# Optimization experiments

Measured on AMD Instinct MI355X. Metric: run time of the kernel, lower is better.

Reference implementation:

```python
import jax, jax.numpy as jnp
import numpy as np

B, S, D = 2, 2048, 1024
H = 16
HD = D // H  # 64
THETA = 10000.0


def apply_rope(x, positions, theta):
    # x: (b, h, s, hd); positions: (s,)
    hd = x.shape[-1]
    inv_freq = theta ** (-jnp.arange(0, hd, 2, dtype=jnp.float32) / hd)  # (hd/2,)
    angles = positions.astype(jnp.float32)[:, None] * inv_freq[None, :]  # (s, hd/2)
    cos, sin = jnp.cos(angles), jnp.sin(angles)
    x1 = x[..., 0::2]
    x2 = x[..., 1::2]
    r1 = x1 * cos - x2 * sin
    r2 = x1 * sin + x2 * cos
    out = jnp.stack([r1, r2], axis=-1).reshape(x.shape)
    return out.astype(x.dtype)


def setup_inputs() -> dict:
    key = jax.random.key(0)
    ks = jax.random.split(key, 5)
    scale = 1.0 / np.sqrt(D)
    return {
        "in_features": jax.random.normal(ks[0], (B, S, D), dtype=jnp.float32),
        "token_positions": jnp.arange(S, dtype=jnp.int32),
        "Wq": jax.random.normal(ks[1], (D, D), dtype=jnp.float32) * scale,
        "Wk": jax.random.normal(ks[2], (D, D), dtype=jnp.float32) * scale,
        "Wv": jax.random.normal(ks[3], (D, D), dtype=jnp.float32) * scale,
        "Wo": jax.random.normal(ks[4], (D, D), dtype=jnp.float32) * scale,
    }


def reference(in_features, token_positions, Wq, Wk, Wv, Wo):
    b, s, d = in_features.shape
    h, hd = H, HD
    # bias-free linear: y = x @ W.T  (W is (out, in))
    q = in_features @ Wq.T
    k = in_features @ Wk.T
    v = in_features @ Wv.T
    # (b, s, h*hd) -> (b, h, s, hd)
    split = lambda t: t.reshape(b, s, h, hd).transpose(0, 2, 1, 3)
    q, k, v = split(q), split(k), split(v)
    q = apply_rope(q, token_positions, THETA)
    k = apply_rope(k, token_positions, THETA)
    scores = jnp.einsum("bhid,bhjd->bhij", q, k) / jnp.sqrt(jnp.asarray(hd, dtype=q.dtype))
    causal = jnp.triu(jnp.ones((s, s), dtype=bool), k=1)
    scores = jnp.where(causal, -jnp.inf, scores)
    attn = jax.nn.softmax(scores, axis=-1)
    out = jnp.einsum("bhij,bhjd->bhid", attn, v)
    out = out.transpose(0, 2, 1, 3).reshape(b, s, d)
    return out @ Wo.T
```

## Files before the change

kernel.cpp:

```cpp
#include <hip/hip_runtime.h>
#include <math.h>

#define NUM_HEADS 16
#define HEAD_DIM 64

typedef __bf16 bf16x8 __attribute__((ext_vector_type(8)));
typedef short shortx4 __attribute__((ext_vector_type(4)));
typedef float floatx4 __attribute__((ext_vector_type(4)));

__device__ __forceinline__ unsigned short f2b(float f) {
  unsigned int u = __float_as_uint(f);
  u += 0x7fffu + ((u >> 16) & 1u);
  return (unsigned short)(u >> 16);
}
__device__ __forceinline__ float b2f(unsigned short s) {
  return __uint_as_float(((unsigned int)s) << 16);
}

__device__ __forceinline__ void async16(const void* g, void* l) {
  __builtin_amdgcn_global_load_lds(
      (const __attribute__((address_space(1))) unsigned int*)g,
      (__attribute__((address_space(3))) unsigned int*)l, 16, 0, 0);
}

__global__ void cvt_f32_bf16(const float* __restrict__ in,
                             unsigned short* __restrict__ out, int n4) {
  int i = blockIdx.x * 256 + threadIdx.x;
  if (i < n4) {
    float4 v = ((const float4*)in)[i];
    ushort4 o;
    o.x = f2b(v.x); o.y = f2b(v.y); o.z = f2b(v.z); o.w = f2b(v.w);
    ((ushort4*)out)[i] = o;
  }
}

__global__ void cvt_w4(const float* __restrict__ w0, const float* __restrict__ w1,
                       const float* __restrict__ w2, const float* __restrict__ w3,
                       unsigned short* o0, unsigned short* o1,
                       unsigned short* o2, unsigned short* o3, int n4) {
  int i = blockIdx.x * 256 + threadIdx.x;
  if (i >= n4) return;
  const float* in = (blockIdx.y == 0) ? w0 : (blockIdx.y == 1) ? w1
                   : (blockIdx.y == 2) ? w2 : w3;
  unsigned short* out = (blockIdx.y == 0) ? o0 : (blockIdx.y == 1) ? o1
                       : (blockIdx.y == 2) ? o2 : o3;
  float4 v = ((const float4*)in)[i];
  ushort4 o;
  o.x = f2b(v.x); o.y = f2b(v.y); o.z = f2b(v.z); o.w = f2b(v.w);
  ((ushort4*)out)[i] = o;
}

__global__ void build_rope_tab(const int* __restrict__ pos,
                               float* __restrict__ tab, int total) {
  int t = blockIdx.x * 256 + threadIdx.x;
  if (t >= total) return;
  int i = t & 31, s = t >> 5;
  float inv = expf(-0.28782313662425575f * (float)i);
  float ang = (float)pos[s] * inv;
  float sn, cs;
  sincosf(ang, &sn, &cs);
  tab[t * 2] = cs;
  tab[t * 2 + 1] = sn;
}

template <int MODE>
__global__ __launch_bounds__(256, 2)
void gemm_bt(const unsigned short* __restrict__ A,
             const unsigned short* __restrict__ B0,
             const unsigned short* __restrict__ B1,
             const unsigned short* __restrict__ B2,
             void* out0v, void* out1v, void* out2v,
             const float* __restrict__ ctab,
             int M, int N, int K, int S) {
  __shared__ unsigned short As[128 * 32];
  __shared__ unsigned short Bs[128 * 32];
  const int tid = threadIdx.x;
  const int lane = tid & 63;
  const int w = tid >> 6;
  const int lane16 = lane & 15;
  const int g = lane >> 4;
  const int wm = w >> 1, wn = w & 1;
  const int m0 = blockIdx.y * 128;
  const int n0 = blockIdx.x * 128;
  const unsigned short* Bp = (blockIdx.z == 0) ? B0 : (blockIdx.z == 1 ? B1 : B2);

  const floatx4 vzero = {0.f, 0.f, 0.f, 0.f};
  floatx4 acc[4][4];
#pragma unroll
  for (int i = 0; i < 4; i++)
#pragma unroll
    for (int j = 0; j < 4; j++) acc[i][j] = vzero;

  const int ar = lane >> 2;
  const int ac = (lane & 3) * 8;

  for (int k0 = 0; k0 < K; k0 += 32) {
#pragma unroll
    for (int c = 0; c < 2; c++) {
      int chunk = w * 2 + c;
      async16(A  + (size_t)(m0 + chunk * 16 + ar) * K + k0 + ac, As + chunk * 512);
      async16(Bp + (size_t)(n0 + chunk * 16 + ar) * K + k0 + ac, Bs + chunk * 512);
    }
    __syncthreads();
    bf16x8 a[4], b[4];
#pragma unroll
    for (int mt = 0; mt < 4; mt++)
      a[mt] = *(const bf16x8*)&As[(wm * 64 + mt * 16 + lane16) * 32 + g * 8];
#pragma unroll
    for (int nt = 0; nt < 4; nt++)
      b[nt] = *(const bf16x8*)&Bs[(wn * 64 + nt * 16 + lane16) * 32 + g * 8];
#pragma unroll
    for (int mt = 0; mt < 4; mt++)
#pragma unroll
      for (int nt = 0; nt < 4; nt++)
        acc[mt][nt] = __builtin_amdgcn_mfma_f32_16x16x32_bf16(b[nt], a[mt], acc[mt][nt], 0, 0, 0);
    __syncthreads();
  }

  if (MODE == 0) {
    unsigned short* outp = (unsigned short*)((blockIdx.z == 0) ? out0v
                              : (blockIdx.z == 1 ? out1v : out2v));
    const bool dorope = (blockIdx.z < 2);
    const float qs = (blockIdx.z == 0) ? 0.125f : 1.0f;
#pragma unroll
    for (int mt = 0; mt < 4; mt++) {
      int m = m0 + wm * 64 + mt * 16 + lane16;
      int bb = m / S, s = m - bb * S;
      const float* crow = ctab + (size_t)s * 64;
#pragma unroll
      for (int nt = 0; nt < 4; nt++) {
        int n = n0 + wn * 64 + nt * 16 + g * 4;
        int h = n >> 6, dl = n & 63;
        floatx4 v = acc[mt][nt];
        if (dorope) {
          float4 cs = *(const float4*)&crow[dl];
          float r0 = (v[0] * cs.x - v[1] * cs.y) * qs;
          float r1 = (v[0] * cs.y + v[1] * cs.x) * qs;
          float r2 = (v[2] * cs.z - v[3] * cs.w) * qs;
          float r3 = (v[2] * cs.w + v[3] * cs.z) * qs;
          v[0] = r0; v[1] = r1; v[2] = r2; v[3] = r3;
        }
        shortx4 st;
#pragma unroll
        for (int r = 0; r < 4; r++) st[r] = (short)f2b(v[r]);
        *(shortx4*)&outp[(((size_t)(bb * NUM_HEADS + h) * S + s) << 6) + dl] = st;
      }
    }
  } else {
    float* outp = (float*)out0v;
#pragma unroll
    for (int mt = 0; mt < 4; mt++) {
      int m = m0 + wm * 64 + mt * 16 + lane16;
#pragma unroll
      for (int nt = 0; nt < 4; nt++) {
        int n = n0 + wn * 64 + nt * 16 + g * 4;
        *(floatx4*)&outp[(size_t)m * N + n] = acc[mt][nt];
      }
    }
  }
}

__global__ __launch_bounds__(256, 4)
void transpose_v(const unsigned short* __restrict__ V,
                 unsigned short* __restrict__ Vt, int S) {
  __shared__ unsigned short t[64 * 72];
  const int tid = threadIdx.x;
  const int lane = tid & 63;
  const int w = tid >> 6;
  const int bh = blockIdx.y;
  const int s0 = blockIdx.x * 64;
  const size_t ibase = (size_t)bh * S * 64;
#pragma unroll
  for (int c = 0; c < 2; ++c) {
    int ch = c * 4 + w;
    union { uint4 v; unsigned short u[8]; } vb;
    vb.v = *(const uint4*)&V[ibase + (size_t)(s0 + lane) * 64 + ch * 8];
#pragma unroll
    for (int e = 0; e < 8; ++e) t[(ch * 8 + e) * 72 + lane] = vb.u[e];
  }
  __syncthreads();
  const size_t obase = (size_t)bh * 64 * S;
#pragma unroll
  for (int c = 0; c < 2; ++c) {
    int idx = c * 256 + tid;
    int d = idx >> 3, sch = idx & 7;
    *(uint4*)&Vt[obase + (size_t)d * S + s0 + sch * 8] = *(const uint4*)&t[d * 72 + sch * 8];
  }
}

__global__ __launch_bounds__(256, 4)
void flash_attn4(const unsigned short* __restrict__ Q,
                 const unsigned short* __restrict__ Kv,
                 const unsigned short* __restrict__ Vt,
                 unsigned short* __restrict__ Oattn, int S) {
  __shared__ unsigned short Ks[2 * 4096];
  __shared__ unsigned short Vs[2 * 4096];
  const int tid = threadIdx.x;
  const int lane = tid & 63;
  const int w = tid >> 6;
  const int lane16 = lane & 15;
  const int g = lane >> 4;
  const int sw = lane16 & 7;
  const int qt = gridDim.x - 1 - blockIdx.x;
  const int bh = blockIdx.y;
  const int b = bh >> 4, h = bh & 15;
  const size_t kbase = (size_t)bh * S * HEAD_DIM;
  const unsigned short* Kbase = Kv + kbase;
  const unsigned short* Vtbase = Vt + (size_t)bh * HEAD_DIM * S;
  const int qrow0 = qt * 64 + w * 16;

  bf16x8 qf0, qf1;
  {
    const unsigned short* qp = Q + kbase + (size_t)(qrow0 + lane16) * HEAD_DIM + g * 8;
    qf0 = *(const bf16x8*)qp;
    qf1 = *(const bf16x8*)(qp + 32);
  }

  const int ci0 = w * 64 + lane;
  const int ci1 = ci0 + 256;
  const int r0 = ci0 >> 3, j0 = (ci0 & 7) ^ (r0 & 7);
  const int r1 = ci1 >> 3, j1 = (ci1 & 7) ^ (r1 & 7);
  const unsigned short* kS0 = Kbase + r0 * HEAD_DIM + j0 * 8;
  const unsigned short* kS1 = Kbase + r1 * HEAD_DIM + j1 * 8;
  const unsigned short* vS0 = Vtbase + (size_t)r0 * S + j0 * 8;
  const unsigned short* vS1 = Vtbase + (size_t)r1 * S + j1 * 8;
  unsigned short* kD0 = Ks + ci0 * 8;
  unsigned short* kD1 = Ks + ci1 * 8;
  unsigned short* vD0 = Vs + ci0 * 8;
  unsigned short* vD1 = Vs + ci1 * 8;

  auto stage = [&](int t, int bi) {
    int koff = t * 4096;
    int voff = t * 64;
    int doff = bi * 4096;
    async16(kS0 + koff, kD0 + doff);
    async16(kS1 + koff, kD1 + doff);
    async16(vS0 + voff, vD0 + doff);
    async16(vS1 + voff, vD1 + doff);
  };

  const floatx4 vzero = {0.f, 0.f, 0.f, 0.f};
  floatx4 oacc[4];
#pragma unroll
  for (int i = 0; i < 4; i++) oacc[i] = vzero;
  float l_i = 0.f;

  stage(0, 0);
  __syncthreads();

  for (int t = 0; t <= qt; ++t) {
    const int bi = t & 1;
    if (t < qt) stage(t + 1, bi ^ 1);
    const unsigned short* Kb_ = Ks + bi * 4096;
    const unsigned short* Vb_ = Vs + bi * 4096;

    floatx4 sc[4];
#pragma unroll
    for (int c = 0; c < 4; ++c) {
      int r = c * 16 + lane16;
      bf16x8 kf0 = *(const bf16x8*)&Kb_[(r * 8 + (g ^ sw)) * 8];
      bf16x8 kf1 = *(const bf16x8*)&Kb_[(r * 8 + ((4 + g) ^ sw)) * 8];
      floatx4 s = vzero;
      s = __builtin_amdgcn_mfma_f32_16x16x32_bf16(kf0, qf0, s, 0, 0, 0);
      s = __builtin_amdgcn_mfma_f32_16x16x32_bf16(kf1, qf1, s, 0, 0, 0);
      sc[c] = s;
    }
    if (t == qt) {
      const int i = qrow0 + lane16;
      const int jb = t * 64;
#pragma unroll
      for (int c = 0; c < 4; ++c)
#pragma unroll
        for (int r = 0; r < 4; ++r)
          if (jb + c * 16 + g * 4 + r > i) sc[c][r] = -INFINITY;
    }
    shortx4 pc[4];
#pragma unroll
    for (int c = 0; c < 4; ++c) {
      float p0 = __expf(sc[c][0]);
      float p1 = __expf(sc[c][1]);
      float p2 = __expf(sc[c][2]);
      float p3 = __expf(sc[c][3]);
      l_i += (p0 + p1) + (p2 + p3);
      union { unsigned int u[2]; shortx4 s4; } pu;
      pu.u[0] = __builtin_amdgcn_perm(__float_as_uint(p1), __float_as_uint(p0), 0x07060302u);
      pu.u[1] = __builtin_amdgcn_perm(__float_as_uint(p3), __float_as_uint(p2), 0x07060302u);
      pc[c] = pu.s4;
    }
#pragma unroll
    for (int nt = 0; nt < 4; ++nt) {
      int rv = nt * 16 + lane16;
#pragma unroll
      for (int c = 0; c < 4; ++c) {
        shortx4 vf = *(const shortx4*)&Vb_[(rv * 8 + ((c * 2 + (g >> 1)) ^ sw)) * 8 + (g & 1) * 4];
        oacc[nt] = __builtin_amdgcn_mfma_f32_16x16x16bf16_1k(vf, pc[c], oacc[nt], 0, 0, 0);
      }
    }
    __syncthreads();
  }

  l_i += __shfl_xor(l_i, 16, 64);
  l_i += __shfl_xor(l_i, 32, 64);
  {
    float inv = 1.0f / l_i;
    int srow = qrow0 + lane16;
    size_t rowb = ((size_t)b * S + srow) * 1024 + h * 64;
#pragma unroll
    for (int nt = 0; nt < 4; ++nt) {
      shortx4 st;
#pragma unroll
      for (int r = 0; r < 4; ++r) st[r] = (short)f2b(oacc[nt][r] * inv);
      *(shortx4*)&Oattn[rowb + nt * 16 + g * 4] = st;
    }
  }
}

extern "C" void kernel_launch(void* const* d_in, const int* in_sizes, int n_in,
                              void* d_out, int out_size, void* d_ws, size_t ws_size,
                              hipStream_t stream) {
  const float* x  = (const float*)d_in[0];
  const int*  pos = (const int*)d_in[1];
  const float* wq = (const float*)d_in[2];
  const float* wk = (const float*)d_in[3];
  const float* wv = (const float*)d_in[4];
  const float* wo = (const float*)d_in[5];

  const int D = 1024;
  const int S = in_sizes[1];
  const int M = in_sizes[0] / D;
  const int B = M / S;
  const int BH = B * NUM_HEADS;

  char* wsb = (char*)d_ws;
  size_t off = 0;
  auto alloc = [&](size_t bytes) {
    char* p = wsb + off;
    off += (bytes + 255) & ~(size_t)255;
    return p;
  };
  unsigned short* Xb   = (unsigned short*)alloc((size_t)M * D * 2);
  unsigned short* Wqb  = (unsigned short*)alloc((size_t)D * D * 2);
  unsigned short* Wkb  = (unsigned short*)alloc((size_t)D * D * 2);
  unsigned short* Wvb  = (unsigned short*)alloc((size_t)D * D * 2);
  unsigned short* Wob  = (unsigned short*)alloc((size_t)D * D * 2);
  unsigned short* Qb   = (unsigned short*)alloc((size_t)M * D * 2);
  unsigned short* Kb   = (unsigned short*)alloc((size_t)M * D * 2);
  unsigned short* Vb   = (unsigned short*)alloc((size_t)M * D * 2);
  unsigned short* Attn = (unsigned short*)alloc((size_t)M * D * 2);
  float*          Ctab = (float*)alloc((size_t)S * 32 * 2 * 4);
  unsigned short* Vtb  = Xb;
  (void)ws_size;

  {
    int n4 = M * D / 4;
    cvt_f32_bf16<<<dim3((n4 + 255) / 256), 256, 0, stream>>>(x, Xb, n4);
    int w4 = D * D / 4;
    cvt_w4<<<dim3((w4 + 255) / 256, 4), 256, 0, stream>>>(
        wq, wk, wv, wo, Wqb, Wkb, Wvb, Wob, w4);
    int tt = S * 32;
    build_rope_tab<<<dim3((tt + 255) / 256), 256, 0, stream>>>(pos, Ctab, tt);
  }
  gemm_bt<0><<<dim3(D / 128, M / 128, 3), 256, 0, stream>>>(
      Xb, Wqb, Wkb, Wvb, Qb, Kb, Vb, Ctab, M, D, D, S);
  transpose_v<<<dim3(S / 64, BH), 256, 0, stream>>>(Vb, Vtb, S);
  flash_attn4<<<dim3(S / 64, BH), 256, 0, stream>>>(Qb, Kb, Vtb, Attn, S);
  gemm_bt<1><<<dim3(D / 128, M / 128, 1), 256, 0, stream>>>(
      Attn, Wob, Wob, Wob, d_out, d_out, d_out, Ctab, M, D, D, S);
}
```

Measured before the change: 204.2 us.

## Fuse prep kernels, double-buffer GEMM with K=64 stages, widen attention blocks

Merges the input, weight and RoPE-table preparation kernels into one launch. The projection GEMM now stages 64-wide K tiles into double-buffered LDS, prefetching the next tile while computing the current one, which halves the number of barriers. The attention kernel moves to 512-thread blocks covering 128 query rows, so each K/V tile load is shared by eight waves. That wider block costs extra causal-masking work near the diagonal, more LDS per block and possible occupancy changes.

New measurement: 219.5 us. 1.08x slower.

```diff
diff --git a/kernel.cpp b/kernel.cpp
--- a/kernel.cpp
+++ b/kernel.cpp
@@ -13,9 +13,6 @@
   u += 0x7fffu + ((u >> 16) & 1u);
   return (unsigned short)(u >> 16);
 }
-__device__ __forceinline__ float b2f(unsigned short s) {
-  return __uint_as_float(((unsigned int)s) << 16);
-}
 
 __device__ __forceinline__ void async16(const void* g, void* l) {
   __builtin_amdgcn_global_load_lds(
@@ -23,44 +20,42 @@
       (__attribute__((address_space(3))) unsigned int*)l, 16, 0, 0);
 }
 
-__global__ void cvt_f32_bf16(const float* __restrict__ in,
-                             unsigned short* __restrict__ out, int n4) {
-  int i = blockIdx.x * 256 + threadIdx.x;
-  if (i < n4) {
-    float4 v = ((const float4*)in)[i];
-    ushort4 o;
-    o.x = f2b(v.x); o.y = f2b(v.y); o.z = f2b(v.z); o.w = f2b(v.w);
-    ((ushort4*)out)[i] = o;
-  }
-}
-
-__global__ void cvt_w4(const float* __restrict__ w0, const float* __restrict__ w1,
-                       const float* __restrict__ w2, const float* __restrict__ w3,
-                       unsigned short* o0, unsigned short* o1,
-                       unsigned short* o2, unsigned short* o3, int n4) {
-  int i = blockIdx.x * 256 + threadIdx.x;
-  if (i >= n4) return;
-  const float* in = (blockIdx.y == 0) ? w0 : (blockIdx.y == 1) ? w1
-                   : (blockIdx.y == 2) ? w2 : w3;
-  unsigned short* out = (blockIdx.y == 0) ? o0 : (blockIdx.y == 1) ? o1
-                       : (blockIdx.y == 2) ? o2 : o3;
+__device__ __forceinline__ void cvt4(const float* in, unsigned short* out, int i) {
   float4 v = ((const float4*)in)[i];
   ushort4 o;
   o.x = f2b(v.x); o.y = f2b(v.y); o.z = f2b(v.z); o.w = f2b(v.w);
   ((ushort4*)out)[i] = o;
 }
 
-__global__ void build_rope_tab(const int* __restrict__ pos,
-                               float* __restrict__ tab, int total) {
-  int t = blockIdx.x * 256 + threadIdx.x;
-  if (t >= total) return;
-  int i = t & 31, s = t >> 5;
-  float inv = expf(-0.28782313662425575f * (float)i);
-  float ang = (float)pos[s] * inv;
-  float sn, cs;
-  sincosf(ang, &sn, &cs);
-  tab[t * 2] = cs;
-  tab[t * 2 + 1] = sn;
+__global__ void prep(const float* __restrict__ x,
+                     const float* __restrict__ w0, const float* __restrict__ w1,
+                     const float* __restrict__ w2, const float* __restrict__ w3,
+                     const int* __restrict__ pos,
+                     unsigned short* Xb, unsigned short* o0, unsigned short* o1,
+                     unsigned short* o2, unsigned short* o3,
+                     float* __restrict__ tab, int w4, int ntab) {
+  int i = blockIdx.x * 256 + threadIdx.x;
+  int z = blockIdx.y;
+  if (z == 0) {
+#pragma unroll
+    for (int rep = 0; rep < 4; ++rep) cvt4(x, Xb, rep * 262144 + i);
+  } else if (z <= 4) {
+    if (i < w4) {
+      const float* in = (z == 1) ? w0 : (z == 2) ? w1 : (z == 3) ? w2 : w3;
+      unsigned short* out = (z == 1) ? o0 : (z == 2) ? o1 : (z == 3) ? o2 : o3;
+      cvt4(in, out, i);
+    }
+  } else {
+    if (i < ntab) {
+      int fi = i & 31, s = i >> 5;
+      float inv = expf(-0.28782313662425575f * (float)fi);
+      float ang = (float)pos[s] * inv;
+      float sn, cs;
+      sincosf(ang, &sn, &cs);
+      tab[i * 2] = cs;
+      tab[i * 2 + 1] = sn;
+    }
+  }
 }
 
 template <int MODE>
@@ -72,8 +67,8 @@
              void* out0v, void* out1v, void* out2v,
              const float* __restrict__ ctab,
              int M, int N, int K, int S) {
-  __shared__ unsigned short As[128 * 32];
-  __shared__ unsigned short Bs[128 * 32];
+  __shared__ unsigned short As[2 * 8192];
+  __shared__ unsigned short Bs[2 * 8192];
   const int tid = threadIdx.x;
   const int lane = tid & 63;
   const int w = tid >> 6;
@@ -93,27 +88,50 @@
 
   const int ar = lane >> 2;
   const int ac = (lane & 3) * 8;
-
-  for (int k0 = 0; k0 < K; k0 += 32) {
-#pragma unroll
-    for (int c = 0; c < 2; c++) {
-      int chunk = w * 2 + c;
-      async16(A  + (size_t)(m0 + chunk * 16 + ar) * K + k0 + ac, As + chunk * 512);
-      async16(Bp + (size_t)(n0 + chunk * 16 + ar) * K + k0 + ac, Bs + chunk * 512);
-    }
-    __syncthreads();
-    bf16x8 a[4], b[4];
-#pragma unroll
-    for (int mt = 0; mt < 4; mt++)
-      a[mt] = *(const bf16x8*)&As[(wm * 64 + mt * 16 + lane16) * 32 + g * 8];
-#pragma unroll
-    for (int nt = 0; nt < 4; nt++)
-      b[nt] = *(const bf16x8*)&Bs[(wn * 64 + nt * 16 + lane16) * 32 + g * 8];
-#pragma unroll
-    for (int mt = 0; mt < 4; mt++)
+  const unsigned short* aS[4];
+  const unsigned short* bS[4];
+  unsigned short* aD[4];
+  unsigned short* bD[4];
+#pragma unroll
+  for (int q = 0; q < 4; ++q) {
+    int ci = w * 4 + q, rc = ci >> 1, kh = ci & 1;
+    aS[q] = A  + (size_t)(m0 + rc * 16 + ar) * K + kh * 32 + ac;
+    bS[q] = Bp + (size_t)(n0 + rc * 16 + ar) * K + kh * 32 + ac;
+    aD[q] = As + ci * 512;
+    bD[q] = Bs + ci * 512;
+  }
+  auto stage = [&](int k0, int bi) {
+    int doff = bi * 8192;
+#pragma unroll
+    for (int q = 0; q < 4; ++q) {
+      async16(aS[q] + k0, aD[q] + doff);
+      async16(bS[q] + k0, bD[q] + doff);
+    }
+  };
+
+  stage(0, 0);
+  __syncthreads();
+
+  for (int k0 = 0; k0 < K; k0 += 64) {
+    const int bi = (k0 >> 6) & 1;
+    if (k0 + 64 < K) stage(k0 + 64, bi ^ 1);
+    const unsigned short* Ab = As + bi * 8192;
+    const unsigned short* Bb = Bs + bi * 8192;
+#pragma unroll
+    for (int kh = 0; kh < 2; ++kh) {
+      bf16x8 a[4], b[4];
+#pragma unroll
+      for (int mt = 0; mt < 4; mt++)
+        a[mt] = *(const bf16x8*)&Ab[((wm * 4 + mt) * 2 + kh) * 512 + lane16 * 32 + g * 8];
 #pragma unroll
       for (int nt = 0; nt < 4; nt++)
-        acc[mt][nt] = __builtin_amdgcn_mfma_f32_16x16x32_bf16(b[nt], a[mt], acc[mt][nt], 0, 0, 0);
+        b[nt] = *(const bf16x8*)&Bb[((wn * 4 + nt) * 2 + kh) * 512 + lane16 * 32 + g * 8];
+#pragma unroll
+      for (int mt = 0; mt < 4; mt++)
+#pragma unroll
+        for (int nt = 0; nt < 4; nt++)
+          acc[mt][nt] = __builtin_amdgcn_mfma_f32_16x16x32_bf16(b[nt], a[mt], acc[mt][nt], 0, 0, 0);
+    }
     __syncthreads();
   }
 
@@ -188,8 +206,8 @@
   }
 }
 
-__global__ __launch_bounds__(256, 4)
-void flash_attn4(const unsigned short* __restrict__ Q,
+__global__ __launch_bounds__(512, 2)
+void flash_attn7(const unsigned short* __restrict__ Q,
                  const unsigned short* __restrict__ Kv,
                  const unsigned short* __restrict__ Vt,
                  unsigned short* __restrict__ Oattn, int S) {
@@ -201,42 +219,33 @@
   const int lane16 = lane & 15;
   const int g = lane >> 4;
   const int sw = lane16 & 7;
-  const int qt = gridDim.x - 1 - blockIdx.x;
+  const int qb = gridDim.x - 1 - blockIdx.x;
   const int bh = blockIdx.y;
   const int b = bh >> 4, h = bh & 15;
   const size_t kbase = (size_t)bh * S * HEAD_DIM;
   const unsigned short* Kbase = Kv + kbase;
   const unsigned short* Vtbase = Vt + (size_t)bh * HEAD_DIM * S;
-  const int qrow0 = qt * 64 + w * 16;
+  const int base = qb * 128 + w * 16;
+  const int diag = (base >> 6);
+  const int tmax = 2 * qb + 1;
 
   bf16x8 qf0, qf1;
   {
-    const unsigned short* qp = Q + kbase + (size_t)(qrow0 + lane16) * HEAD_DIM + g * 8;
+    const unsigned short* qp = Q + kbase + (size_t)(base + lane16) * HEAD_DIM + g * 8;
     qf0 = *(const bf16x8*)qp;
     qf1 = *(const bf16x8*)(qp + 32);
   }
 
-  const int ci0 = w * 64 + lane;
-  const int ci1 = ci0 + 256;
-  const int r0 = ci0 >> 3, j0 = (ci0 & 7) ^ (r0 & 7);
-  const int r1 = ci1 >> 3, j1 = (ci1 & 7) ^ (r1 & 7);
-  const unsigned short* kS0 = Kbase + r0 * HEAD_DIM + j0 * 8;
-  const unsigned short* kS1 = Kbase + r1 * HEAD_DIM + j1 * 8;
-  const unsigned short* vS0 = Vtbase + (size_t)r0 * S + j0 * 8;
-  const unsigned short* vS1 = Vtbase + (size_t)r1 * S + j1 * 8;
-  unsigned short* kD0 = Ks + ci0 * 8;
-  unsigned short* kD1 = Ks + ci1 * 8;
-  unsigned short* vD0 = Vs + ci0 * 8;
-  unsigned short* vD1 = Vs + ci1 * 8;
+  const int ci = tid;
+  const int r0 = ci >> 3, j0 = (ci & 7) ^ (r0 & 7);
+  const unsigned short* kS = Kbase + r0 * HEAD_DIM + j0 * 8;
+  const unsigned short* vS = Vtbase + (size_t)r0 * S + j0 * 8;
+  unsigned short* kD = Ks + ci * 8;
+  unsigned short* vD = Vs + ci * 8;
 
   auto stage = [&](int t, int bi) {
-    int koff = t * 4096;
-    int voff = t * 64;
-    int doff = bi * 4096;
-    async16(kS0 + koff, kD0 + doff);
-    async16(kS1 + koff, kD1 + doff);
-    async16(vS0 + voff, vD0 + doff);
-    async16(vS1 + voff, vD1 + doff);
+    async16(kS + t * 4096, kD + bi * 4096);
+    async16(vS + t * 64, vD + bi * 4096);
   };
 
   const floatx4 vzero = {0.f, 0.f, 0.f, 0.f};
@@ -248,9 +257,9 @@
   stage(0, 0);
   __syncthreads();
 
-  for (int t = 0; t <= qt; ++t) {
+  for (int t = 0; t <= tmax; ++t) {
     const int bi = t & 1;
-    if (t < qt) stage(t + 1, bi ^ 1);
+    if (t < tmax) stage(t + 1, bi ^ 1);
     const unsigned short* Kb_ = Ks + bi * 4096;
     const unsigned short* Vb_ = Vs + bi * 4096;
 
@@ -265,8 +274,8 @@
       s = __builtin_amdgcn_mfma_f32_16x16x32_bf16(kf1, qf1, s, 0, 0, 0);
       sc[c] = s;
     }
-    if (t == qt) {
-      const int i = qrow0 + lane16;
+    if (t >= diag) {
+      const int i = base + lane16;
       const int jb = t * 64;
 #pragma unroll
       for (int c = 0; c < 4; ++c)
@@ -303,7 +312,7 @@
   l_i += __shfl_xor(l_i, 32, 64);
   {
     float inv = 1.0f / l_i;
-    int srow = qrow0 + lane16;
+    int srow = base + lane16;
     size_t rowb = ((size_t)b * S + srow) * 1024 + h * 64;
 #pragma unroll
     for (int nt = 0; nt < 4; ++nt) {
@@ -352,18 +361,16 @@
   (void)ws_size;
 
   {
-    int n4 = M * D / 4;
-    cvt_f32_bf16<<<dim3((n4 + 255) / 256), 256, 0, stream>>>(x, Xb, n4);
     int w4 = D * D / 4;
-    cvt_w4<<<dim3((w4 + 255) / 256, 4), 256, 0, stream>>>(
-        wq, wk, wv, wo, Wqb, Wkb, Wvb, Wob, w4);
-    int tt = S * 32;
-    build_rope_tab<<<dim3((tt + 255) / 256), 256, 0, stream>>>(pos, Ctab, tt);
+    int ntab = S * 32;
+    prep<<<dim3(1024, 6), 256, 0, stream>>>(x, wq, wk, wv, wo, pos,
+                                            Xb, Wqb, Wkb, Wvb, Wob, Ctab,
+                                            w4, ntab);
   }
   gemm_bt<0><<<dim3(D / 128, M / 128, 3), 256, 0, stream>>>(
       Xb, Wqb, Wkb, Wvb, Qb, Kb, Vb, Ctab, M, D, D, S);
   transpose_v<<<dim3(S / 64, BH), 256, 0, stream>>>(Vb, Vtb, S);
-  flash_attn4<<<dim3(S / 64, BH), 256, 0, stream>>>(Qb, Kb, Vtb, Attn, S);
+  flash_attn7<<<dim3(S / 128, BH), 512, 0, stream>>>(Qb, Kb, Vtb, Attn, S);
   gemm_bt<1><<<dim3(D / 128, M / 128, 1), 256, 0, stream>>>(
       Attn, Wob, Wob, Wob, d_out, d_out, d_out, Ctab, M, D, D, S);
 }
```

## Fuse prep kernels, write V transposed from GEMM, use 64-row tiles for output GEMM

Applied to the files above, without the earlier changes.

Folds the input/weight bf16 conversions and RoPE table build into a single prep kernel to cut launch count. The QKV GEMM epilogue now writes V directly in transposed (d-major) layout, which removes the separate transpose kernel, at the cost of scalar strided 2-byte stores. The output projection GEMM uses 64-row tiles with higher occupancy bounds so more blocks cover the 256 CUs.

After: 192.8 us. 5.6% less time.

```diff
diff --git a/kernel.cpp b/kernel.cpp
--- a/kernel.cpp
+++ b/kernel.cpp
@@ -13,9 +13,6 @@
   u += 0x7fffu + ((u >> 16) & 1u);
   return (unsigned short)(u >> 16);
 }
-__device__ __forceinline__ float b2f(unsigned short s) {
-  return __uint_as_float(((unsigned int)s) << 16);
-}
 
 __device__ __forceinline__ void async16(const void* g, void* l) {
   __builtin_amdgcn_global_load_lds(
@@ -23,48 +20,48 @@
       (__attribute__((address_space(3))) unsigned int*)l, 16, 0, 0);
 }
 
-__global__ void cvt_f32_bf16(const float* __restrict__ in,
-                             unsigned short* __restrict__ out, int n4) {
-  int i = blockIdx.x * 256 + threadIdx.x;
-  if (i < n4) {
-    float4 v = ((const float4*)in)[i];
-    ushort4 o;
-    o.x = f2b(v.x); o.y = f2b(v.y); o.z = f2b(v.z); o.w = f2b(v.w);
-    ((ushort4*)out)[i] = o;
-  }
-}
-
-__global__ void cvt_w4(const float* __restrict__ w0, const float* __restrict__ w1,
-                       const float* __restrict__ w2, const float* __restrict__ w3,
-                       unsigned short* o0, unsigned short* o1,
-                       unsigned short* o2, unsigned short* o3, int n4) {
-  int i = blockIdx.x * 256 + threadIdx.x;
-  if (i >= n4) return;
-  const float* in = (blockIdx.y == 0) ? w0 : (blockIdx.y == 1) ? w1
-                   : (blockIdx.y == 2) ? w2 : w3;
-  unsigned short* out = (blockIdx.y == 0) ? o0 : (blockIdx.y == 1) ? o1
-                       : (blockIdx.y == 2) ? o2 : o3;
+__device__ __forceinline__ void cvt4(const float* in, unsigned short* out, int i) {
   float4 v = ((const float4*)in)[i];
   ushort4 o;
   o.x = f2b(v.x); o.y = f2b(v.y); o.z = f2b(v.z); o.w = f2b(v.w);
   ((ushort4*)out)[i] = o;
 }
 
-__global__ void build_rope_tab(const int* __restrict__ pos,
-                               float* __restrict__ tab, int total) {
-  int t = blockIdx.x * 256 + threadIdx.x;
-  if (t >= total) return;
-  int i = t & 31, s = t >> 5;
-  float inv = expf(-0.28782313662425575f * (float)i);
-  float ang = (float)pos[s] * inv;
-  float sn, cs;
-  sincosf(ang, &sn, &cs);
-  tab[t * 2] = cs;
-  tab[t * 2 + 1] = sn;
-}
-
-template <int MODE>
-__global__ __launch_bounds__(256, 2)
+__global__ void prep(const float* __restrict__ x,
+                     const float* __restrict__ w0, const float* __restrict__ w1,
+                     const float* __restrict__ w2, const float* __restrict__ w3,
+                     const int* __restrict__ pos,
+                     unsigned short* Xb, unsigned short* o0, unsigned short* o1,
+                     unsigned short* o2, unsigned short* o3,
+                     float* __restrict__ tab, int xq, int w4, int ntab) {
+  int i = blockIdx.x * 256 + threadIdx.x;
+  int z = blockIdx.y;
+  if (z == 0) {
+    if (i < xq) {
+#pragma unroll
+      for (int rep = 0; rep < 4; ++rep) cvt4(x, Xb, rep * xq + i);
+    }
+  } else if (z <= 4) {
+    if (i < w4) {
+      const float* in = (z == 1) ? w0 : (z == 2) ? w1 : (z == 3) ? w2 : w3;
+      unsigned short* out = (z == 1) ? o0 : (z == 2) ? o1 : (z == 3) ? o2 : o3;
+      cvt4(in, out, i);
+    }
+  } else {
+    if (i < ntab) {
+      int fi = i & 31, s = i >> 5;
+      float inv = expf(-0.28782313662425575f * (float)fi);
+      float ang = (float)pos[s] * inv;
+      float sn, cs;
+      sincosf(ang, &sn, &cs);
+      tab[i * 2] = cs;
+      tab[i * 2 + 1] = sn;
+    }
+  }
+}
+
+template <int MODE, int MT>
+__global__ __launch_bounds__(256, MODE == 1 ? 4 : 2)
 void gemm_bt(const unsigned short* __restrict__ A,
              const unsigned short* __restrict__ B0,
              const unsigned short* __restrict__ B1,
@@ -72,22 +69,23 @@
              void* out0v, void* out1v, void* out2v,
              const float* __restrict__ ctab,
              int M, int N, int K, int S) {
-  __shared__ unsigned short As[128 * 32];
-  __shared__ unsigned short Bs[128 * 32];
+  __shared__ unsigned short As[(MT / 16) * 512];
+  __shared__ unsigned short Bs[8 * 512];
   const int tid = threadIdx.x;
   const int lane = tid & 63;
   const int w = tid >> 6;
   const int lane16 = lane & 15;
   const int g = lane >> 4;
   const int wm = w >> 1, wn = w & 1;
-  const int m0 = blockIdx.y * 128;
+  const int m0 = blockIdx.y * MT;
   const int n0 = blockIdx.x * 128;
   const unsigned short* Bp = (blockIdx.z == 0) ? B0 : (blockIdx.z == 1 ? B1 : B2);
+  constexpr int MTILES = MT / 32;
 
   const floatx4 vzero = {0.f, 0.f, 0.f, 0.f};
-  floatx4 acc[4][4];
-#pragma unroll
-  for (int i = 0; i < 4; i++)
+  floatx4 acc[MTILES][4];
+#pragma unroll
+  for (int i = 0; i < MTILES; i++)
 #pragma unroll
     for (int j = 0; j < 4; j++) acc[i][j] = vzero;
 
@@ -95,22 +93,28 @@
   const int ac = (lane & 3) * 8;
 
   for (int k0 = 0; k0 < K; k0 += 32) {
-#pragma unroll
-    for (int c = 0; c < 2; c++) {
-      int chunk = w * 2 + c;
-      async16(A  + (size_t)(m0 + chunk * 16 + ar) * K + k0 + ac, As + chunk * 512);
-      async16(Bp + (size_t)(n0 + chunk * 16 + ar) * K + k0 + ac, Bs + chunk * 512);
+    if constexpr (MT == 128) {
+#pragma unroll
+      for (int c = 0; c < 2; c++) {
+        int chunk = w * 2 + c;
+        async16(A  + (size_t)(m0 + chunk * 16 + ar) * K + k0 + ac, As + chunk * 512);
+        async16(Bp + (size_t)(n0 + chunk * 16 + ar) * K + k0 + ac, Bs + chunk * 512);
+      }
+    } else {
+      async16(A  + (size_t)(m0 + w * 16 + ar) * K + k0 + ac, As + w * 512);
+      async16(Bp + (size_t)(n0 + w * 16 + ar) * K + k0 + ac, Bs + w * 512);
+      async16(Bp + (size_t)(n0 + (w + 4) * 16 + ar) * K + k0 + ac, Bs + (w + 4) * 512);
     }
     __syncthreads();
-    bf16x8 a[4], b[4];
-#pragma unroll
-    for (int mt = 0; mt < 4; mt++)
-      a[mt] = *(const bf16x8*)&As[(wm * 64 + mt * 16 + lane16) * 32 + g * 8];
+    bf16x8 a[MTILES], b[4];
+#pragma unroll
+    for (int mt = 0; mt < MTILES; mt++)
+      a[mt] = *(const bf16x8*)&As[(wm * (MT / 2) + mt * 16 + lane16) * 32 + g * 8];
 #pragma unroll
     for (int nt = 0; nt < 4; nt++)
       b[nt] = *(const bf16x8*)&Bs[(wn * 64 + nt * 16 + lane16) * 32 + g * 8];
 #pragma unroll
-    for (int mt = 0; mt < 4; mt++)
+    for (int mt = 0; mt < MTILES; mt++)
 #pragma unroll
       for (int nt = 0; nt < 4; nt++)
         acc[mt][nt] = __builtin_amdgcn_mfma_f32_16x16x32_bf16(b[nt], a[mt], acc[mt][nt], 0, 0, 0);
@@ -118,73 +122,59 @@
   }
 
   if (MODE == 0) {
-    unsigned short* outp = (unsigned short*)((blockIdx.z == 0) ? out0v
-                              : (blockIdx.z == 1 ? out1v : out2v));
-    const bool dorope = (blockIdx.z < 2);
-    const float qs = (blockIdx.z == 0) ? 0.125f : 1.0f;
-#pragma unroll
-    for (int mt = 0; mt < 4; mt++) {
-      int m = m0 + wm * 64 + mt * 16 + lane16;
-      int bb = m / S, s = m - bb * S;
-      const float* crow = ctab + (size_t)s * 64;
-#pragma unroll
-      for (int nt = 0; nt < 4; nt++) {
-        int n = n0 + wn * 64 + nt * 16 + g * 4;
-        int h = n >> 6, dl = n & 63;
-        floatx4 v = acc[mt][nt];
-        if (dorope) {
+    if (blockIdx.z < 2) {
+      unsigned short* outp = (unsigned short*)((blockIdx.z == 0) ? out0v : out1v);
+      const float qs = (blockIdx.z == 0) ? 0.125f : 1.0f;
+#pragma unroll
+      for (int mt = 0; mt < MTILES; mt++) {
+        int m = m0 + wm * (MT / 2) + mt * 16 + lane16;
+        int bb = m / S, s = m - bb * S;
+        const float* crow = ctab + (size_t)s * 64;
+#pragma unroll
+        for (int nt = 0; nt < 4; nt++) {
+          int n = n0 + wn * 64 + nt * 16 + g * 4;
+          int h = n >> 6, dl = n & 63;
+          floatx4 v = acc[mt][nt];
           float4 cs = *(const float4*)&crow[dl];
           float r0 = (v[0] * cs.x - v[1] * cs.y) * qs;
           float r1 = (v[0] * cs.y + v[1] * cs.x) * qs;
           float r2 = (v[2] * cs.z - v[3] * cs.w) * qs;
           float r3 = (v[2] * cs.w + v[3] * cs.z) * qs;
-          v[0] = r0; v[1] = r1; v[2] = r2; v[3] = r3;
+          shortx4 st;
+          st[0] = (short)f2b(r0); st[1] = (short)f2b(r1);
+          st[2] = (short)f2b(r2); st[3] = (short)f2b(r3);
+          *(shortx4*)&outp[(((size_t)(bb * NUM_HEADS + h) * S + s) << 6) + dl] = st;
         }
-        shortx4 st;
-#pragma unroll
-        for (int r = 0; r < 4; r++) st[r] = (short)f2b(v[r]);
-        *(shortx4*)&outp[(((size_t)(bb * NUM_HEADS + h) * S + s) << 6) + dl] = st;
+      }
+    } else {
+      unsigned short* outp = (unsigned short*)out2v;
+#pragma unroll
+      for (int mt = 0; mt < MTILES; mt++) {
+        int m = m0 + wm * (MT / 2) + mt * 16 + lane16;
+        int bb = m / S, s = m - bb * S;
+#pragma unroll
+        for (int nt = 0; nt < 4; nt++) {
+          int n = n0 + wn * 64 + nt * 16 + g * 4;
+          int bh = bb * NUM_HEADS + (n >> 6);
+          int dl = n & 63;
+          size_t dbase = ((size_t)bh * 64 + dl) * S + s;
+#pragma unroll
+          for (int r = 0; r < 4; r++)
+            outp[dbase + (size_t)r * S] = f2b(acc[mt][nt][r]);
+        }
       }
     }
   } else {
     float* outp = (float*)out0v;
 #pragma unroll
-    for (int mt = 0; mt < 4; mt++) {
-      int m = m0 + wm * 64 + mt * 16 + lane16;
+    for (int mt = 0; mt < MTILES; mt++) {
+      int m = m0 + wm * (MT / 2) + mt * 16 + lane16;
 #pragma unroll
       for (int nt = 0; nt < 4; nt++) {
         int n = n0 + wn * 64 + nt * 16 + g * 4;
         *(floatx4*)&outp[(size_t)m * N + n] = acc[mt][nt];
       }
     }
-  }
-}
-
-__global__ __launch_bounds__(256, 4)
-void transpose_v(const unsigned short* __restrict__ V,
-                 unsigned short* __restrict__ Vt, int S) {
-  __shared__ unsigned short t[64 * 72];
-  const int tid = threadIdx.x;
-  const int lane = tid & 63;
-  const int w = tid >> 6;
-  const int bh = blockIdx.y;
-  const int s0 = blockIdx.x * 64;
-  const size_t ibase = (size_t)bh * S * 64;
-#pragma unroll
-  for (int c = 0; c < 2; ++c) {
-    int ch = c * 4 + w;
-    union { uint4 v; unsigned short u[8]; } vb;
-    vb.v = *(const uint4*)&V[ibase + (size_t)(s0 + lane) * 64 + ch * 8];
-#pragma unroll
-    for (int e = 0; e < 8; ++e) t[(ch * 8 + e) * 72 + lane] = vb.u[e];
-  }
-  __syncthreads();
-  const size_t obase = (size_t)bh * 64 * S;
-#pragma unroll
-  for (int c = 0; c < 2; ++c) {
-    int idx = c * 256 + tid;
-    int d = idx >> 3, sch = idx & 7;
-    *(uint4*)&Vt[obase + (size_t)d * S + s0 + sch * 8] = *(const uint4*)&t[d * 72 + sch * 8];
   }
 }
 
@@ -345,25 +335,24 @@
   unsigned short* Wob  = (unsigned short*)alloc((size_t)D * D * 2);
   unsigned short* Qb   = (unsigned short*)alloc((size_t)M * D * 2);
   unsigned short* Kb   = (unsigned short*)alloc((size_t)M * D * 2);
-  unsigned short* Vb   = (unsigned short*)alloc((size_t)M * D * 2);
+  unsigned short* Vtb  = (unsigned short*)alloc((size_t)M * D * 2);
   unsigned short* Attn = (unsigned short*)alloc((size_t)M * D * 2);
   float*          Ctab = (float*)alloc((size_t)S * 32 * 2 * 4);
-  unsigned short* Vtb  = Xb;
   (void)ws_size;
 
   {
-    int n4 = M * D / 4;
-    cvt_f32_bf16<<<dim3((n4 + 255) / 256), 256, 0, stream>>>(x, Xb, n4);
+    int n4x = M * D / 4;
+    int xq = n4x / 4;
     int w4 = D * D / 4;
-    cvt_w4<<<dim3((w4 + 255) / 256, 4), 256, 0, stream>>>(
-        wq, wk, wv, wo, Wqb, Wkb, Wvb, Wob, w4);
-    int tt = S * 32;
-    build_rope_tab<<<dim3((tt + 255) / 256), 256, 0, stream>>>(pos, Ctab, tt);
-  }
-  gemm_bt<0><<<dim3(D / 128, M / 128, 3), 256, 0, stream>>>(
-      Xb, Wqb, Wkb, Wvb, Qb, Kb, Vb, Ctab, M, D, D, S);
-  transpose_v<<<dim3(S / 64, BH), 256, 0, stream>>>(Vb, Vtb, S);
+    int ntab = S * 32;
+    int gx = (w4 + 255) / 256;
+    prep<<<dim3(gx, 6), 256, 0, stream>>>(x, wq, wk, wv, wo, pos,
+                                          Xb, Wqb, Wkb, Wvb, Wob, Ctab,
+                                          xq, w4, ntab);
+  }
+  gemm_bt<0, 128><<<dim3(D / 128, M / 128, 3), 256, 0, stream>>>(
+      Xb, Wqb, Wkb, Wvb, Qb, Kb, Vtb, Ctab, M, D, D, S);
   flash_attn4<<<dim3(S / 64, BH), 256, 0, stream>>>(Qb, Kb, Vtb, Attn, S);
-  gemm_bt<1><<<dim3(D / 128, M / 128, 1), 256, 0, stream>>>(
+  gemm_bt<1, 64><<<dim3(D / 128, M / 64, 1), 256, 0, stream>>>(
       Attn, Wob, Wob, Wob, d_out, d_out, d_out, Ctab, M, D, D, S);
 }
```
